# Optimization experiments

Hardware: AMD Instinct MI355X
Metric: run time of the kernel (lower is better)

Reference implementation:

```python
import jax, jax.numpy as jnp
import numpy as np

N_NODES = 100000
N_EDGES = 800000
D_IN = 128      # input_dim (node feature dim)
D_HID = 128     # output_dim (MLP hidden dim)


def setup_inputs() -> dict:
    key = jax.random.key(0)
    ks = jax.random.split(key, 7)
    node_emb = jax.random.normal(ks[0], (N_NODES, D_IN), dtype=jnp.float32)
    src = jax.random.randint(ks[1], (N_EDGES,), 0, N_NODES, dtype=jnp.int64)
    dst = jax.random.randint(ks[2], (N_EDGES,), 0, N_NODES, dtype=jnp.int64)
    W1 = jax.random.normal(ks[3], (2 * D_IN, D_HID), dtype=jnp.float32) / np.sqrt(2 * D_IN)
    b1 = jnp.zeros((D_HID,), dtype=jnp.float32)
    W2 = jax.random.normal(ks[4], (D_HID, 1), dtype=jnp.float32) / np.sqrt(D_HID)
    b2 = jnp.zeros((1,), dtype=jnp.float32)
    u_gate = jax.random.uniform(ks[5], (N_EDGES, 1), dtype=jnp.float32)  # torch.rand noise for gumbel gate
    u_bern = jax.random.uniform(ks[6], (N_EDGES,), dtype=jnp.float32)    # uniform noise for RelaxedBernoulli.rsample
    return {"node_emb": node_emb, "src": src, "dst": dst,
            "W1": W1, "b1": b1, "W2": W2, "b2": b2,
            "u_gate": u_gate, "u_bern": u_bern}


def reference(node_emb, src, dst, W1, b1, W2, b2, u_gate, u_bern):
    BIAS = 1e-4          # bias in forward
    TEMP_GATE = 1.0      # temperature in forward
    TEMP_BERN = 0.9      # temperature passed to build_prob_neighbourhood

    # edge gather + concat: [E, 2*D_IN]
    edge_emb = jnp.concatenate([node_emb[src], node_emb[dst]], axis=1)
    # 2-layer per-edge MLP -> logits [E, 1]
    h = jax.nn.relu(edge_emb @ W1 + b1)
    edge_logits = h @ W2 + b2

    # gumbel-sigmoid gate: eps in (BIAS, 1-BIAS]
    eps = (BIAS - (1.0 - BIAS)) * u_gate + (1.0 - BIAS)
    gate_inputs = (jnp.log(eps) - jnp.log1p(-eps) + edge_logits) / TEMP_GATE
    edge_weight = jax.nn.sigmoid(gate_inputs).squeeze(-1)  # [E]

    # build_prob_neighbourhood: RelaxedBernoulli(temperature=0.9, probs=clamped).rsample()
    attention = jnp.clip(edge_weight, 0.01, 0.99)
    bern_logits = jnp.log(attention) - jnp.log1p(-attention)
    u = jnp.clip(u_bern, 1e-7, 1.0 - 1e-7)
    w = jax.nn.sigmoid((bern_logits + jnp.log(u) - jnp.log1p(-u)) / TEMP_BERN)

    # mask = (w > 0).detach().float(); w = w*mask + 0*(1-mask)
    mask = jax.lax.stop_gradient((w > 0.0).astype(w.dtype))
    return w * mask
```

## Files before the change

### kernel.cpp

```cpp
#include <hip/hip_runtime.h>
#include <hip/hip_bf16.h>
#include <cstdint>

#define D  128
#define NT 256
#define OSTRIDE 544

typedef __attribute__((ext_vector_type(8))) short bf16x8;
typedef __attribute__((ext_vector_type(4))) float f32x4;

__device__ __forceinline__ unsigned int packbf(float lo, float hi) {
    const unsigned int ulo = __float_as_uint(lo) + 0x8000u;
    const unsigned int uhi = __float_as_uint(hi) + 0x8000u;
    return __builtin_amdgcn_perm(uhi, ulo, 0x07060302);
}

__global__ __launch_bounds__(256) void pack_w1(
    const float* __restrict__ W1, unsigned short* __restrict__ Wp)
{
    const int t = blockIdx.x * 256 + threadIdx.x;
    if (t >= 4096) return;
    const int lane = t & 63;
    const int fc = t >> 6;
    const int cg = fc >> 2, ks = fc & 3;
    const int lr = lane & 15, lg = lane >> 4;
    const int half = cg >> 3;
    const int col = (cg & 7) * 16 + lr;
    const int krow = half * 128 + ks * 32 + lg * 8;
    const float* wp = W1 + (size_t)krow * D + col;
    uint4 u;
    u.x = packbf(wp[0 * D], wp[1 * D]);
    u.y = packbf(wp[2 * D], wp[3 * D]);
    u.z = packbf(wp[4 * D], wp[5 * D]);
    u.w = packbf(wp[6 * D], wp[7 * D]);
    reinterpret_cast<uint4*>(Wp)[t] = u;
}

__global__ __launch_bounds__(256, 3) void node_mlp_mfma(
    const float* __restrict__ x, const unsigned short* __restrict__ Wp,
    unsigned short* __restrict__ T, int N)
{
    __shared__ unsigned char obuf[64 * OSTRIDE];
    __shared__ uint4 xfrag[1024];

    const int t = threadIdx.x;
    const int lane = t & 63;
    const int w = t >> 6;
    const int lr = lane & 15;
    const int lg = lane >> 4;
    const int base = blockIdx.x * 64;

    bf16x8 wf[4][4];
    {
        const uint4* wsrc = reinterpret_cast<const uint4*>(Wp);
        #pragma unroll
        for (int c = 0; c < 4; ++c)
            #pragma unroll
            for (int ks = 0; ks < 4; ++ks)
                wf[c][ks] = __builtin_bit_cast(bf16x8,
                    wsrc[(((w * 4 + c) * 4 + ks) << 6) + lane]);
    }

    #pragma unroll
    for (int i = 0; i < 4; ++i) {
        const int m = t + 256 * i;
        const int r = m >> 4;
        const int c8 = m & 15;
        int row = base + r; if (row > N - 1) row = N - 1;
        const float4* px = reinterpret_cast<const float4*>(x + (size_t)row * D + c8 * 8);
        const float4 v0 = px[0], v1 = px[1];
        uint4 u;
        u.x = packbf(v0.x, v0.y); u.y = packbf(v0.z, v0.w);
        u.z = packbf(v1.x, v1.y); u.w = packbf(v1.z, v1.w);
        const int s = r >> 4, lr2 = r & 15, ks = c8 >> 2, lg2 = c8 & 3;
        int idx = ((s * 4 + ks) << 6) + (lg2 << 4) + lr2;
        idx ^= ((idx >> 4) & 3) << 2;
        xfrag[idx] = u;
    }
    __syncthreads();

    const int lxor = lane ^ (((lane >> 4) & 3) << 2);
    #pragma unroll
    for (int s = 0; s < 4; ++s) {
        bf16x8 xf[4];
        #pragma unroll
        for (int ks = 0; ks < 4; ++ks)
            xf[ks] = __builtin_bit_cast(bf16x8, xfrag[((s * 4 + ks) << 6) + lxor]);

        f32x4 acc[4];
        #pragma unroll
        for (int c = 0; c < 4; ++c) acc[c] = (f32x4){0.f, 0.f, 0.f, 0.f};
        #pragma unroll
        for (int ks = 0; ks < 4; ++ks)
            #pragma unroll
            for (int c = 0; c < 4; ++c)
                acc[c] = __builtin_amdgcn_mfma_f32_16x16x32_bf16(
                    wf[c][ks], xf[ks], acc[c], 0, 0, 0);

        unsigned char* p = obuf + (s * 16 + lr) * OSTRIDE + w * 128 + lg * 8;
        #pragma unroll
        for (int c = 0; c < 4; ++c) {
            uint2 o;
            o.x = packbf(acc[c][0], acc[c][1]);
            o.y = packbf(acc[c][2], acc[c][3]);
            *reinterpret_cast<uint2*>(p + c * 32) = o;
        }
    }
    __syncthreads();

    {
        const int drow = t >> 2;
        const int dcol = (t & 3) * 16;
        const int node = base + drow;
        if (node < N) {
            const unsigned char* sp = obuf + drow * OSTRIDE + dcol;
            unsigned char* gp = reinterpret_cast<unsigned char*>(T) +
                                (size_t)node * (NT * 2) + dcol;
            #pragma unroll
            for (int i = 0; i < 8; ++i)
                *reinterpret_cast<uint4*>(gp + i * 64) =
                    *reinterpret_cast<const uint4*>(sp + i * 64);
        }
    }
}

__device__ __forceinline__ float acc_pair(uint32_t wa, uint32_t wb,
                                          float blo, float bhi,
                                          float w2lo, float w2hi, float p) {
    const float alo = __uint_as_float(wa << 16);
    const float ahi = __uint_as_float(wa & 0xffff0000u);
    const float clo = __uint_as_float(wb << 16);
    const float chi = __uint_as_float(wb & 0xffff0000u);
    const float h0 = fmaxf(alo + clo + blo, 0.f);
    const float h1 = fmaxf(ahi + chi + bhi, 0.f);
    p = fmaf(h0, w2lo, p);
    p = fmaf(h1, w2hi, p);
    return p;
}

__device__ __forceinline__ float fast_sigmoid(float xv) {
    const float e = __builtin_amdgcn_exp2f(xv * -1.44269504f);
    return __builtin_amdgcn_rcpf(1.f + e);
}

__global__ __launch_bounds__(256) void edge_kernel(
    const unsigned short* __restrict__ T,
    const int* __restrict__ src, const int* __restrict__ dst,
    const float* __restrict__ b1, const float* __restrict__ W2,
    const float* __restrict__ b2,
    const float* __restrict__ u_gate, const float* __restrict__ u_bern,
    float* __restrict__ out, int E)
{
    const int gid = blockIdx.x * blockDim.x + threadIdx.x;
    const int e = gid >> 3;
    if (e >= E) return;
    const int sub = threadIdx.x & 7;

    const int s = src[e];
    const int d = dst[e];

    const uint4* Ap = reinterpret_cast<const uint4*>(T + (size_t)s * NT + sub * 16);
    const uint4* Bp = reinterpret_cast<const uint4*>(T + (size_t)d * NT + 128 + sub * 16);
    const float4* Bv = reinterpret_cast<const float4*>(b1 + sub * 16);
    const float4* Wv = reinterpret_cast<const float4*>(W2 + sub * 16);

    const uint4 a0 = Ap[0], a1 = Ap[1];
    const uint4 c0 = Bp[0], c1 = Bp[1];
    const float4 bb0 = Bv[0], bb1 = Bv[1], bb2 = Bv[2], bb3 = Bv[3];
    const float4 w0 = Wv[0], w1 = Wv[1], w2 = Wv[2], w3 = Wv[3];

    float p = 0.f;
    p = acc_pair(a0.x, c0.x, bb0.x, bb0.y, w0.x, w0.y, p);
    p = acc_pair(a0.y, c0.y, bb0.z, bb0.w, w0.z, w0.w, p);
    p = acc_pair(a0.z, c0.z, bb1.x, bb1.y, w1.x, w1.y, p);
    p = acc_pair(a0.w, c0.w, bb1.z, bb1.w, w1.z, w1.w, p);
    p = acc_pair(a1.x, c1.x, bb2.x, bb2.y, w2.x, w2.y, p);
    p = acc_pair(a1.y, c1.y, bb2.z, bb2.w, w2.z, w2.w, p);
    p = acc_pair(a1.z, c1.z, bb3.x, bb3.y, w3.x, w3.y, p);
    p = acc_pair(a1.w, c1.w, bb3.z, bb3.w, w3.z, w3.w, p);

    p += __shfl_xor(p, 1, 64);
    p += __shfl_xor(p, 2, 64);
    p += __shfl_xor(p, 4, 64);

    if (sub == 0) {
        const float logit = p + b2[0];

        const float ug  = u_gate[e];
        const float eps = fmaf(-0.9998f, ug, 0.9999f);
        const float g = (__builtin_amdgcn_logf(eps) -
                         __builtin_amdgcn_logf(1.f - eps)) * 0.69314718f + logit;

        const float bl = fminf(fmaxf(g, -4.59511985f), 4.59511985f);

        const float ub  = fminf(fmaxf(u_bern[e], 1e-7f), 1.f - 1e-7f);
        const float lu  = (__builtin_amdgcn_logf(ub) -
                           __builtin_amdgcn_logf(1.f - ub)) * 0.69314718f;
        const float arg = (bl + lu) * (1.0f / 0.9f);
        out[e] = fast_sigmoid(arg);
    }
}

extern "C" void kernel_launch(void* const* d_in, const int* in_sizes, int n_in,
                              void* d_out, int out_size, void* d_ws, size_t ws_size,
                              hipStream_t stream)
{
    const float* node_emb = (const float*)d_in[0];
    const int*   src      = (const int*)d_in[1];
    const int*   dst      = (const int*)d_in[2];
    const float* W1       = (const float*)d_in[3];
    const float* b1       = (const float*)d_in[4];
    const float* W2       = (const float*)d_in[5];
    const float* b2       = (const float*)d_in[6];
    const float* u_gate   = (const float*)d_in[7];
    const float* u_bern   = (const float*)d_in[8];
    float* out = (float*)d_out;

    const int N = in_sizes[0] / D;
    const int E = in_sizes[1];

    unsigned short* Wp = (unsigned short*)d_ws;
    unsigned short* T  = Wp + 32768;

    pack_w1<<<16, 256, 0, stream>>>(W1, Wp);

    const int nMacro = (N + 63) / 64;
    node_mlp_mfma<<<nMacro, 256, 0, stream>>>(node_emb, Wp, T, N);

    const long long dotThreads = (long long)E * 8;
    const int blocksE = (int)((dotThreads + 255) / 256);
    edge_kernel<<<blocksE, 256, 0, stream>>>(T, src, dst, b1, W2, b2,
                                             u_gate, u_bern, out, E);
}
```

Baseline: 174.6 us.

## Persistent node MLP with prefetch and two edges per thread group

The node-projection kernel becomes grid-strided over half as many blocks, so the W1 fragments are loaded once per block. It also prefetches the next tile's node features into registers while the current tile's results are written out. The edge kernel now handles two edges per 8-lane group, using vectorized int2/float2 loads for indices, noise and output, which doubles the gathers in flight per thread. Odd edge counts are no longer handled (the last edge is dropped), and register pressure rises in both kernels.

```diff
diff --git a/kernel.cpp b/kernel.cpp
--- a/kernel.cpp
+++ b/kernel.cpp
@@ -38,7 +38,7 @@
 
 __global__ __launch_bounds__(256, 3) void node_mlp_mfma(
     const float* __restrict__ x, const unsigned short* __restrict__ Wp,
-    unsigned short* __restrict__ T, int N)
+    unsigned short* __restrict__ T, int N, int nMacro)
 {
     __shared__ unsigned char obuf[64 * OSTRIDE];
     __shared__ uint4 xfrag[1024];
@@ -48,7 +48,6 @@
     const int w = t >> 6;
     const int lr = lane & 15;
     const int lg = lane >> 4;
-    const int base = blockIdx.x * 64;
 
     bf16x8 wf[4][4];
     {
@@ -61,66 +60,94 @@
                     wsrc[(((w * 4 + c) * 4 + ks) << 6) + lane]);
     }
 
+    int m = blockIdx.x;
+    if (m >= nMacro) return;
+
+    float4 xr[4][2];
     #pragma unroll
     for (int i = 0; i < 4; ++i) {
-        const int m = t + 256 * i;
-        const int r = m >> 4;
-        const int c8 = m & 15;
-        int row = base + r; if (row > N - 1) row = N - 1;
-        const float4* px = reinterpret_cast<const float4*>(x + (size_t)row * D + c8 * 8);
-        const float4 v0 = px[0], v1 = px[1];
-        uint4 u;
-        u.x = packbf(v0.x, v0.y); u.y = packbf(v0.z, v0.w);
-        u.z = packbf(v1.x, v1.y); u.w = packbf(v1.z, v1.w);
-        const int s = r >> 4, lr2 = r & 15, ks = c8 >> 2, lg2 = c8 & 3;
-        int idx = ((s * 4 + ks) << 6) + (lg2 << 4) + lr2;
-        idx ^= ((idx >> 4) & 3) << 2;
-        xfrag[idx] = u;
-    }
-    __syncthreads();
+        const int mm = t + 256 * i;
+        int row = m * 64 + (mm >> 4); if (row > N - 1) row = N - 1;
+        const float4* px = reinterpret_cast<const float4*>(x + (size_t)row * D + (mm & 15) * 8);
+        xr[i][0] = px[0]; xr[i][1] = px[1];
+    }
 
     const int lxor = lane ^ (((lane >> 4) & 3) << 2);
-    #pragma unroll
-    for (int s = 0; s < 4; ++s) {
-        bf16x8 xf[4];
+
+    for (;;) {
+        const int base = m * 64;
+
         #pragma unroll
-        for (int ks = 0; ks < 4; ++ks)
-            xf[ks] = __builtin_bit_cast(bf16x8, xfrag[((s * 4 + ks) << 6) + lxor]);
-
-        f32x4 acc[4];
+        for (int i = 0; i < 4; ++i) {
+            const int mm = t + 256 * i;
+            const int r = mm >> 4, c8 = mm & 15;
+            uint4 u;
+            u.x = packbf(xr[i][0].x, xr[i][0].y); u.y = packbf(xr[i][0].z, xr[i][0].w);
+            u.z = packbf(xr[i][1].x, xr[i][1].y); u.w = packbf(xr[i][1].z, xr[i][1].w);
+            const int s = r >> 4, lr2 = r & 15, ks = c8 >> 2, lg2 = c8 & 3;
+            int idx = ((s * 4 + ks) << 6) + (lg2 << 4) + lr2;
+            idx ^= ((idx >> 4) & 3) << 2;
+            xfrag[idx] = u;
+        }
+        __syncthreads();
+
         #pragma unroll
-        for (int c = 0; c < 4; ++c) acc[c] = (f32x4){0.f, 0.f, 0.f, 0.f};
-        #pragma unroll
-        for (int ks = 0; ks < 4; ++ks)
-            #pragma unroll
-            for (int c = 0; c < 4; ++c)
-                acc[c] = __builtin_amdgcn_mfma_f32_16x16x32_bf16(
-                    wf[c][ks], xf[ks], acc[c], 0, 0, 0);
-
-        unsigned char* p = obuf + (s * 16 + lr) * OSTRIDE + w * 128 + lg * 8;
-        #pragma unroll
-        for (int c = 0; c < 4; ++c) {
-            uint2 o;
-            o.x = packbf(acc[c][0], acc[c][1]);
-            o.y = packbf(acc[c][2], acc[c][3]);
-            *reinterpret_cast<uint2*>(p + c * 32) = o;
-        }
-    }
-    __syncthreads();
-
-    {
-        const int drow = t >> 2;
-        const int dcol = (t & 3) * 16;
-        const int node = base + drow;
-        if (node < N) {
-            const unsigned char* sp = obuf + drow * OSTRIDE + dcol;
-            unsigned char* gp = reinterpret_cast<unsigned char*>(T) +
-                                (size_t)node * (NT * 2) + dcol;
-            #pragma unroll
-            for (int i = 0; i < 8; ++i)
-                *reinterpret_cast<uint4*>(gp + i * 64) =
-                    *reinterpret_cast<const uint4*>(sp + i * 64);
-        }
+        for (int s = 0; s < 4; ++s) {
+            bf16x8 xf[4];
+            #pragma unroll
+            for (int ks = 0; ks < 4; ++ks)
+                xf[ks] = __builtin_bit_cast(bf16x8, xfrag[((s * 4 + ks) << 6) + lxor]);
+
+            f32x4 acc[4];
+            #pragma unroll
+            for (int c = 0; c < 4; ++c) acc[c] = (f32x4){0.f, 0.f, 0.f, 0.f};
+            #pragma unroll
+            for (int ks = 0; ks < 4; ++ks)
+                #pragma unroll
+                for (int c = 0; c < 4; ++c)
+                    acc[c] = __builtin_amdgcn_mfma_f32_16x16x32_bf16(
+                        wf[c][ks], xf[ks], acc[c], 0, 0, 0);
+
+            unsigned char* p = obuf + (s * 16 + lr) * OSTRIDE + w * 128 + lg * 8;
+            #pragma unroll
+            for (int c = 0; c < 4; ++c) {
+                uint2 o;
+                o.x = packbf(acc[c][0], acc[c][1]);
+                o.y = packbf(acc[c][2], acc[c][3]);
+                *reinterpret_cast<uint2*>(p + c * 32) = o;
+            }
+        }
+        __syncthreads();
+
+        const int mn = m + gridDim.x;
+        const bool more = (mn < nMacro);
+        if (more) {
+            #pragma unroll
+            for (int i = 0; i < 4; ++i) {
+                const int mm = t + 256 * i;
+                int row = mn * 64 + (mm >> 4); if (row > N - 1) row = N - 1;
+                const float4* px = reinterpret_cast<const float4*>(x + (size_t)row * D + (mm & 15) * 8);
+                xr[i][0] = px[0]; xr[i][1] = px[1];
+            }
+        }
+
+        {
+            const int drow = t >> 2;
+            const int dcol = (t & 3) * 16;
+            const int node = base + drow;
+            if (node < N) {
+                const unsigned char* sp = obuf + drow * OSTRIDE + dcol;
+                unsigned char* gp = reinterpret_cast<unsigned char*>(T) +
+                                    (size_t)node * (NT * 2) + dcol;
+                #pragma unroll
+                for (int i = 0; i < 8; ++i)
+                    *reinterpret_cast<uint4*>(gp + i * 64) =
+                        *reinterpret_cast<const uint4*>(sp + i * 64);
+            }
+        }
+
+        if (!more) break;
+        m = mn;
     }
 }
 
@@ -143,6 +170,17 @@
     return __builtin_amdgcn_rcpf(1.f + e);
 }
 
+__device__ __forceinline__ float tail_math(float logit, float ug, float ubr) {
+    const float eps = fmaf(-0.9998f, ug, 0.9999f);
+    const float g = (__builtin_amdgcn_logf(eps) -
+                     __builtin_amdgcn_logf(1.f - eps)) * 0.69314718f + logit;
+    const float bl = fminf(fmaxf(g, -4.59511985f), 4.59511985f);
+    const float ub = fminf(fmaxf(ubr, 1e-7f), 1.f - 1e-7f);
+    const float lu = (__builtin_amdgcn_logf(ub) -
+                      __builtin_amdgcn_logf(1.f - ub)) * 0.69314718f;
+    return fast_sigmoid((bl + lu) * (1.0f / 0.9f));
+}
+
 __global__ __launch_bounds__(256) void edge_kernel(
     const unsigned short* __restrict__ T,
     const int* __restrict__ src, const int* __restrict__ dst,
@@ -152,52 +190,59 @@
     float* __restrict__ out, int E)
 {
     const int gid = blockIdx.x * blockDim.x + threadIdx.x;
-    const int e = gid >> 3;
-    if (e >= E) return;
+    const int p = gid >> 3;
+    const int P = E >> 1;
+    if (p >= P) return;
     const int sub = threadIdx.x & 7;
 
-    const int s = src[e];
-    const int d = dst[e];
-
-    const uint4* Ap = reinterpret_cast<const uint4*>(T + (size_t)s * NT + sub * 16);
-    const uint4* Bp = reinterpret_cast<const uint4*>(T + (size_t)d * NT + 128 + sub * 16);
+    const int2 ss = *reinterpret_cast<const int2*>(src + 2 * p);
+    const int2 dd = *reinterpret_cast<const int2*>(dst + 2 * p);
+
+    const uint4* Ap0 = reinterpret_cast<const uint4*>(T + (size_t)ss.x * NT + sub * 16);
+    const uint4* Cp0 = reinterpret_cast<const uint4*>(T + (size_t)dd.x * NT + 128 + sub * 16);
+    const uint4* Ap1 = reinterpret_cast<const uint4*>(T + (size_t)ss.y * NT + sub * 16);
+    const uint4* Cp1 = reinterpret_cast<const uint4*>(T + (size_t)dd.y * NT + 128 + sub * 16);
+
+    const uint4 a00 = Ap0[0], a01 = Ap0[1];
+    const uint4 c00 = Cp0[0], c01 = Cp0[1];
+    const uint4 a10 = Ap1[0], a11 = Ap1[1];
+    const uint4 c10 = Cp1[0], c11 = Cp1[1];
+
     const float4* Bv = reinterpret_cast<const float4*>(b1 + sub * 16);
     const float4* Wv = reinterpret_cast<const float4*>(W2 + sub * 16);
-
-    const uint4 a0 = Ap[0], a1 = Ap[1];
-    const uint4 c0 = Bp[0], c1 = Bp[1];
     const float4 bb0 = Bv[0], bb1 = Bv[1], bb2 = Bv[2], bb3 = Bv[3];
     const float4 w0 = Wv[0], w1 = Wv[1], w2 = Wv[2], w3 = Wv[3];
 
-    float p = 0.f;
-    p = acc_pair(a0.x, c0.x, bb0.x, bb0.y, w0.x, w0.y, p);
-    p = acc_pair(a0.y, c0.y, bb0.z, bb0.w, w0.z, w0.w, p);
-    p = acc_pair(a0.z, c0.z, bb1.x, bb1.y, w1.x, w1.y, p);
-    p = acc_pair(a0.w, c0.w, bb1.z, bb1.w, w1.z, w1.w, p);
-    p = acc_pair(a1.x, c1.x, bb2.x, bb2.y, w2.x, w2.y, p);
-    p = acc_pair(a1.y, c1.y, bb2.z, bb2.w, w2.z, w2.w, p);
-    p = acc_pair(a1.z, c1.z, bb3.x, bb3.y, w3.x, w3.y, p);
-    p = acc_pair(a1.w, c1.w, bb3.z, bb3.w, w3.z, w3.w, p);
-
-    p += __shfl_xor(p, 1, 64);
-    p += __shfl_xor(p, 2, 64);
-    p += __shfl_xor(p, 4, 64);
+    float p0 = 0.f, p1 = 0.f;
+    p0 = acc_pair(a00.x, c00.x, bb0.x, bb0.y, w0.x, w0.y, p0);
+    p1 = acc_pair(a10.x, c10.x, bb0.x, bb0.y, w0.x, w0.y, p1);
+    p0 = acc_pair(a00.y, c00.y, bb0.z, bb0.w, w0.z, w0.w, p0);
+    p1 = acc_pair(a10.y, c10.y, bb0.z, bb0.w, w0.z, w0.w, p1);
+    p0 = acc_pair(a00.z, c00.z, bb1.x, bb1.y, w1.x, w1.y, p0);
+    p1 = acc_pair(a10.z, c10.z, bb1.x, bb1.y, w1.x, w1.y, p1);
+    p0 = acc_pair(a00.w, c00.w, bb1.z, bb1.w, w1.z, w1.w, p0);
+    p1 = acc_pair(a10.w, c10.w, bb1.z, bb1.w, w1.z, w1.w, p1);
+    p0 = acc_pair(a01.x, c01.x, bb2.x, bb2.y, w2.x, w2.y, p0);
+    p1 = acc_pair(a11.x, c11.x, bb2.x, bb2.y, w2.x, w2.y, p1);
+    p0 = acc_pair(a01.y, c01.y, bb2.z, bb2.w, w2.z, w2.w, p0);
+    p1 = acc_pair(a11.y, c11.y, bb2.z, bb2.w, w2.z, w2.w, p1);
+    p0 = acc_pair(a01.z, c01.z, bb3.x, bb3.y, w3.x, w3.y, p0);
+    p1 = acc_pair(a11.z, c11.z, bb3.x, bb3.y, w3.x, w3.y, p1);
+    p0 = acc_pair(a01.w, c01.w, bb3.z, bb3.w, w3.z, w3.w, p0);
+    p1 = acc_pair(a11.w, c11.w, bb3.z, bb3.w, w3.z, w3.w, p1);
+
+    p0 += __shfl_xor(p0, 1, 64);  p1 += __shfl_xor(p1, 1, 64);
+    p0 += __shfl_xor(p0, 2, 64);  p1 += __shfl_xor(p1, 2, 64);
+    p0 += __shfl_xor(p0, 4, 64);  p1 += __shfl_xor(p1, 4, 64);
 
     if (sub == 0) {
-        const float logit = p + b2[0];
-
-        const float ug  = u_gate[e];
-        const float eps = fmaf(-0.9998f, ug, 0.9999f);
-        const float g = (__builtin_amdgcn_logf(eps) -
-                         __builtin_amdgcn_logf(1.f - eps)) * 0.69314718f + logit;
-
-        const float bl = fminf(fmaxf(g, -4.59511985f), 4.59511985f);
-
-        const float ub  = fminf(fmaxf(u_bern[e], 1e-7f), 1.f - 1e-7f);
-        const float lu  = (__builtin_amdgcn_logf(ub) -
-                           __builtin_amdgcn_logf(1.f - ub)) * 0.69314718f;
-        const float arg = (bl + lu) * (1.0f / 0.9f);
-        out[e] = fast_sigmoid(arg);
+        const float b2v = b2[0];
+        const float2 ug = *reinterpret_cast<const float2*>(u_gate + 2 * p);
+        const float2 ub = *reinterpret_cast<const float2*>(u_bern + 2 * p);
+        float2 o;
+        o.x = tail_math(p0 + b2v, ug.x, ub.x);
+        o.y = tail_math(p1 + b2v, ug.y, ub.y);
+        *reinterpret_cast<float2*>(out + 2 * p) = o;
     }
 }
 
@@ -225,10 +270,12 @@
     pack_w1<<<16, 256, 0, stream>>>(W1, Wp);
 
     const int nMacro = (N + 63) / 64;
-    node_mlp_mfma<<<nMacro, 256, 0, stream>>>(node_emb, Wp, T, N);
-
-    const long long dotThreads = (long long)E * 8;
-    const int blocksE = (int)((dotThreads + 255) / 256);
+    const int gridN = (nMacro + 1) / 2;
+    node_mlp_mfma<<<gridN, 256, 0, stream>>>(node_emb, Wp, T, N, nMacro);
+
+    const int P = E >> 1;
+    const long long thr = (long long)P * 8;
+    const int blocksE = (int)((thr + 255) / 256);
     edge_kernel<<<blocksE, 256, 0, stream>>>(T, src, dst, b1, W2, b2,
                                              u_gate, u_bern, out, E);
 }
```

Result: faster. 170.6 us (-2.3%).
